# Kernel tuning notes

Measured on AMD Instinct MI355X. Metric: run time of the kernel, lower is better.

Reference implementation:

```python
import jax, jax.numpy as jnp
import numpy as np

B, T, S, D, K = 512, 49, 200, 512, 128


def setup_inputs() -> dict:
    key = jax.random.key(0)
    ks = jax.random.split(key, 8)
    return {
        "ifeature": jax.random.normal(ks[0], (B, T, D), dtype=jnp.float32),
        "tfeature_h": jax.random.normal(ks[1], (B, S, D), dtype=jnp.float32),
        "w_Dense_Vi_0": jax.random.normal(ks[2], (D, K), dtype=jnp.float32) * 0.05,
        "w_Dense_Vt_0": jax.random.normal(ks[3], (D, K), dtype=jnp.float32) * 0.05,
        "w_Dense_Pi_0": jax.random.normal(ks[4], (2 * K, 1), dtype=jnp.float32) * 0.05,
        "b_Dense_Pi_0": jnp.zeros((T,), dtype=jnp.float32),
        "w_Dense_Vi_1": jax.random.normal(ks[5], (D, K), dtype=jnp.float32) * 0.05,
        "w_Dense_Vt_1": jax.random.normal(ks[6], (D, K), dtype=jnp.float32) * 0.05,
        "w_Dense_Pi_1": jax.random.normal(ks[7], (2 * K, 1), dtype=jnp.float32) * 0.05,
        "b_Dense_Pi_1": jnp.zeros((S,), dtype=jnp.float32),
    }


def reference(ifeature, tfeature_h, w_Dense_Vi_0, w_Dense_Vt_0, w_Dense_Pi_0,
              b_Dense_Pi_0, w_Dense_Vi_1, w_Dense_Vt_1, w_Dense_Pi_1, b_Dense_Pi_1):
    # tfeature: mean-pooled text, [B, D]
    tfeature = jnp.mean(tfeature_h, axis=1)

    # --- attention over image regions (title_len) ---
    w_Vi_0 = jnp.einsum('btd,dk->btk', ifeature, w_Dense_Vi_0)          # [B,T,K]
    w_Vt_0 = (tfeature @ w_Dense_Vt_0)[:, None, :]                      # [B,1,K] broadcast to T
    Hi = jnp.tanh(jnp.concatenate(
        [w_Vi_0, jnp.broadcast_to(w_Vt_0, w_Vi_0.shape)], axis=-1))     # [B,T,2K]
    Hi_w_b = jnp.einsum('btk,k->bt', Hi, w_Dense_Pi_0[:, 0]) + b_Dense_Pi_0
    Pi = jax.nn.softmax(Hi_w_b, axis=-1)                                # [B,T]
    Vi = jnp.einsum('bt,btd->bd', Pi, ifeature)                         # attended image feature

    # --- attention over text tokens (seq_len) ---
    w_Vi_1 = (Vi @ w_Dense_Vi_1)[:, None, :]                            # [B,1,K]
    w_Vt_1 = jnp.einsum('bsd,dk->bsk', tfeature_h, w_Dense_Vt_1)        # [B,S,K]
    Ht = jnp.tanh(jnp.concatenate(
        [jnp.broadcast_to(w_Vi_1, w_Vt_1.shape), w_Vt_1], axis=-1))     # [B,S,2K]
    Ht_b = jnp.einsum('bsk,k->bs', Ht, w_Dense_Pi_1[:, 0]) + b_Dense_Pi_1
    Pt = jax.nn.softmax(Ht_b, axis=-1)                                  # [B,S]

    # NOTE: original call() returns Pt_Vt (weighted tokens), not the pooled Vt.
    Pt_Vt = Pt[:, :, None] * tfeature_h                                 # [B,S,D]
    return Pt_Vt
```

## Files before the change

kernel.cpp:

```cpp
#include <hip/hip_runtime.h>
#include <math.h>

#define BB 512
#define SS 200
#define DD 512
#define KK 128

typedef __attribute__((ext_vector_type(8))) short bf16x8;
typedef __attribute__((ext_vector_type(4))) float f32x4;

__device__ inline unsigned short f2bf(float f) {
    union { float f; unsigned int u; } v; v.f = f;
    unsigned int r = v.u + 0x7FFFu + ((v.u >> 16) & 1u);
    return (unsigned short)(r >> 16);
}

__device__ inline bf16x8 pack8(const float4& a, const float4& b) {
    bf16x8 p;
    p[0] = (short)f2bf(a.x); p[1] = (short)f2bf(a.y);
    p[2] = (short)f2bf(a.z); p[3] = (short)f2bf(a.w);
    p[4] = (short)f2bf(b.x); p[5] = (short)f2bf(b.y);
    p[6] = (short)f2bf(b.z); p[7] = (short)f2bf(b.w);
    return p;
}

__global__ void wt_kernel(const float* __restrict__ W, unsigned short* __restrict__ Wt) {
    int i = blockIdx.x * 256 + threadIdx.x;
    int col = i >> 9, d = i & 511;
    Wt[i] = f2bf(W[d * KK + col]);
}

__global__ __launch_bounds__(512, 4) void fused_kernel(
    const float* __restrict__ tfh,
    const unsigned short* __restrict__ Wt,
    const float* __restrict__ wpk,
    const float* __restrict__ bias,
    float* __restrict__ out)
{
    __shared__ unsigned short Bs[2][KK][40];
    __shared__ float logit_s[256];
    __shared__ float Pt[SS];
    __shared__ float wpart[8];

    int tid = threadIdx.x;
    int w   = tid >> 6;
    int l   = tid & 63;
    int l15 = l & 15;
    int g   = l >> 4;
    int b   = blockIdx.x;
    const float* Ab = tfh + (size_t)b * SS * DD;

    int row0 = w * 32 + l15;
    int row1 = row0 + 16;
    bool v0 = row0 < SS, v1 = row1 < SS;
    const float* a0 = Ab + (size_t)row0 * DD + g * 8;
    const float* a1 = Ab + (size_t)row1 * DD + g * 8;

    int brow = tid >> 2;
    int bcol = (tid & 3) * 8;
    const unsigned short* bp = Wt + (size_t)brow * DD + bcol;

    f32x4 acc[2][8];
    #pragma unroll
    for (int m = 0; m < 2; ++m)
        #pragma unroll
        for (int n = 0; n < 8; ++n) acc[m][n] = (f32x4){0.f, 0.f, 0.f, 0.f};

    float wv[8];
    #pragma unroll
    for (int n = 0; n < 8; ++n) wv[n] = wpk[n * 16 + l15];

    const float4 fz = make_float4(0.f, 0.f, 0.f, 0.f);

    float4 cA00 = v0 ? *(const float4*)(a0)     : fz;
    float4 cA01 = v0 ? *(const float4*)(a0 + 4) : fz;
    float4 cA10 = v1 ? *(const float4*)(a1)     : fz;
    float4 cA11 = v1 ? *(const float4*)(a1 + 4) : fz;
    *(bf16x8*)&Bs[0][brow][bcol] = *(const bf16x8*)(bp);
    __syncthreads();

    #pragma unroll 2
    for (int t = 0; t < 16; ++t) {
        int p = t & 1;
        float4 nA00, nA01, nA10, nA11;
        bf16x8 nB;
        if (t < 15) {
            int d = (t + 1) * 32;
            nA00 = v0 ? *(const float4*)(a0 + d)     : fz;
            nA01 = v0 ? *(const float4*)(a0 + d + 4) : fz;
            nA10 = v1 ? *(const float4*)(a1 + d)     : fz;
            nA11 = v1 ? *(const float4*)(a1 + d + 4) : fz;
            nB   = *(const bf16x8*)(bp + d);
        }
        bf16x8 af0 = pack8(cA00, cA01);
        bf16x8 af1 = pack8(cA10, cA11);
        #pragma unroll
        for (int n = 0; n < 8; ++n) {
            bf16x8 bfv = *(const bf16x8*)&Bs[p][n * 16 + l15][g * 8];
            acc[0][n] = __builtin_amdgcn_mfma_f32_16x16x32_bf16(af0, bfv, acc[0][n], 0, 0, 0);
            acc[1][n] = __builtin_amdgcn_mfma_f32_16x16x32_bf16(af1, bfv, acc[1][n], 0, 0, 0);
        }
        if (t < 15) *(bf16x8*)&Bs[p ^ 1][brow][bcol] = nB;
        __syncthreads();
        cA00 = nA00; cA01 = nA01; cA10 = nA10; cA11 = nA11;
    }

    float rs[2][4];
    #pragma unroll
    for (int m = 0; m < 2; ++m)
        #pragma unroll
        for (int r = 0; r < 4; ++r) rs[m][r] = 0.f;
    #pragma unroll
    for (int m = 0; m < 2; ++m)
        #pragma unroll
        for (int n = 0; n < 8; ++n)
            #pragma unroll
            for (int r = 0; r < 4; ++r)
                rs[m][r] += tanhf(acc[m][n][r]) * wv[n];
    #pragma unroll
    for (int m = 0; m < 2; ++m)
        #pragma unroll
        for (int r = 0; r < 4; ++r) {
            float v = rs[m][r];
            v += __shfl_xor(v, 1, 64);
            v += __shfl_xor(v, 2, 64);
            v += __shfl_xor(v, 4, 64);
            v += __shfl_xor(v, 8, 64);
            rs[m][r] = v;
        }
    if (l15 == 0) {
        #pragma unroll
        for (int m = 0; m < 2; ++m)
            #pragma unroll
            for (int r = 0; r < 4; ++r) {
                int srow = w * 32 + m * 16 + g * 4 + r;
                if (srow < SS) logit_s[srow] = rs[m][r] + bias[srow];
            }
    }
    __syncthreads();

    float v = (tid < SS) ? logit_s[tid] : -INFINITY;
    float m = v;
    #pragma unroll
    for (int off = 32; off > 0; off >>= 1) m = fmaxf(m, __shfl_xor(m, off, 64));
    if (l == 0) wpart[w] = m;
    __syncthreads();
    m = -INFINITY;
    #pragma unroll
    for (int i = 0; i < 8; ++i) m = fmaxf(m, wpart[i]);
    float e = (tid < SS) ? expf(v - m) : 0.f;
    float ssum = e;
    #pragma unroll
    for (int off = 32; off > 0; off >>= 1) ssum += __shfl_xor(ssum, off, 64);
    __syncthreads();
    if (l == 0) wpart[w] = ssum;
    __syncthreads();
    ssum = 0.f;
    #pragma unroll
    for (int i = 0; i < 8; ++i) ssum += wpart[i];
    if (tid < SS) Pt[tid] = e / ssum;
    __syncthreads();

    const float4* src = (const float4*)Ab;
    float4*       dst = (float4*)(out + (size_t)b * SS * DD);
    const int n4 = SS * DD / 4;
    for (int i = tid; i < n4; i += 512) {
        float p = Pt[i >> 7];
        float4 x = src[i];
        x.x *= p; x.y *= p; x.z *= p; x.w *= p;
        dst[i] = x;
    }
}

extern "C" void kernel_launch(void* const* d_in, const int* in_sizes, int n_in,
                              void* d_out, int out_size, void* d_ws, size_t ws_size,
                              hipStream_t stream) {
    const float* tfh   = (const float*)d_in[1];
    const float* wVt1  = (const float*)d_in[7];
    const float* wp1   = (const float*)d_in[8];
    const float* bias1 = (const float*)d_in[9];
    float* out = (float*)d_out;

    unsigned short* Wt = (unsigned short*)d_ws;

    wt_kernel<<<KK * DD / 256, 256, 0, stream>>>(wVt1, Wt);
    fused_kernel<<<BB, 512, 0, stream>>>(tfh, Wt, wp1 + KK, bias1, out);
}
```

Measured before the change: 141.1 us.

## Pre-swizzle weights into MFMA fragment order and load B directly from global

Result: slower. 153.1 us (+8.5%).

```diff
diff --git a/kernel.cpp b/kernel.cpp
--- a/kernel.cpp
+++ b/kernel.cpp
@@ -24,20 +24,24 @@
     return p;
 }
 
-__global__ void wt_kernel(const float* __restrict__ W, unsigned short* __restrict__ Wt) {
+__global__ void wt_kernel(const float* __restrict__ W, unsigned short* __restrict__ Wt2) {
     int i = blockIdx.x * 256 + threadIdx.x;
-    int col = i >> 9, d = i & 511;
-    Wt[i] = f2bf(W[d * KK + col]);
+    int j = i & 7;
+    int l = (i >> 3) & 63;
+    int n = (i >> 9) & 7;
+    int t = i >> 12;
+    int k = n * 16 + (l & 15);
+    int d = t * 32 + (l >> 4) * 8 + j;
+    Wt2[i] = f2bf(W[d * KK + k]);
 }
 
 __global__ __launch_bounds__(512, 4) void fused_kernel(
     const float* __restrict__ tfh,
-    const unsigned short* __restrict__ Wt,
+    const unsigned short* __restrict__ Wt2,
     const float* __restrict__ wpk,
     const float* __restrict__ bias,
     float* __restrict__ out)
 {
-    __shared__ unsigned short Bs[2][KK][40];
     __shared__ float logit_s[256];
     __shared__ float Pt[SS];
     __shared__ float wpart[8];
@@ -55,20 +59,13 @@
     bool v0 = row0 < SS, v1 = row1 < SS;
     const float* a0 = Ab + (size_t)row0 * DD + g * 8;
     const float* a1 = Ab + (size_t)row1 * DD + g * 8;
-
-    int brow = tid >> 2;
-    int bcol = (tid & 3) * 8;
-    const unsigned short* bp = Wt + (size_t)brow * DD + bcol;
+    const unsigned short* bp = Wt2 + (size_t)l * 8;
 
     f32x4 acc[2][8];
     #pragma unroll
     for (int m = 0; m < 2; ++m)
         #pragma unroll
         for (int n = 0; n < 8; ++n) acc[m][n] = (f32x4){0.f, 0.f, 0.f, 0.f};
-
-    float wv[8];
-    #pragma unroll
-    for (int n = 0; n < 8; ++n) wv[n] = wpk[n * 16 + l15];
 
     const float4 fz = make_float4(0.f, 0.f, 0.f, 0.f);
 
@@ -76,34 +73,54 @@
     float4 cA01 = v0 ? *(const float4*)(a0 + 4) : fz;
     float4 cA10 = v1 ? *(const float4*)(a1)     : fz;
     float4 cA11 = v1 ? *(const float4*)(a1 + 4) : fz;
-    *(bf16x8*)&Bs[0][brow][bcol] = *(const bf16x8*)(bp);
-    __syncthreads();
 
     #pragma unroll 2
     for (int t = 0; t < 16; ++t) {
-        int p = t & 1;
         float4 nA00, nA01, nA10, nA11;
-        bf16x8 nB;
         if (t < 15) {
             int d = (t + 1) * 32;
             nA00 = v0 ? *(const float4*)(a0 + d)     : fz;
             nA01 = v0 ? *(const float4*)(a0 + d + 4) : fz;
             nA10 = v1 ? *(const float4*)(a1 + d)     : fz;
             nA11 = v1 ? *(const float4*)(a1 + d + 4) : fz;
-            nB   = *(const bf16x8*)(bp + d);
         }
         bf16x8 af0 = pack8(cA00, cA01);
         bf16x8 af1 = pack8(cA10, cA11);
-        #pragma unroll
-        for (int n = 0; n < 8; ++n) {
-            bf16x8 bfv = *(const bf16x8*)&Bs[p][n * 16 + l15][g * 8];
-            acc[0][n] = __builtin_amdgcn_mfma_f32_16x16x32_bf16(af0, bfv, acc[0][n], 0, 0, 0);
-            acc[1][n] = __builtin_amdgcn_mfma_f32_16x16x32_bf16(af1, bfv, acc[1][n], 0, 0, 0);
-        }
-        if (t < 15) *(bf16x8*)&Bs[p ^ 1][brow][bcol] = nB;
-        __syncthreads();
+        const unsigned short* bt = bp + (size_t)t * (8 * 64 * 8);
+        {
+            bf16x8 b0 = *(const bf16x8*)(bt);
+            bf16x8 b1 = *(const bf16x8*)(bt + 1 * 512);
+            bf16x8 b2 = *(const bf16x8*)(bt + 2 * 512);
+            bf16x8 b3 = *(const bf16x8*)(bt + 3 * 512);
+            acc[0][0] = __builtin_amdgcn_mfma_f32_16x16x32_bf16(af0, b0, acc[0][0], 0, 0, 0);
+            acc[1][0] = __builtin_amdgcn_mfma_f32_16x16x32_bf16(af1, b0, acc[1][0], 0, 0, 0);
+            acc[0][1] = __builtin_amdgcn_mfma_f32_16x16x32_bf16(af0, b1, acc[0][1], 0, 0, 0);
+            acc[1][1] = __builtin_amdgcn_mfma_f32_16x16x32_bf16(af1, b1, acc[1][1], 0, 0, 0);
+            acc[0][2] = __builtin_amdgcn_mfma_f32_16x16x32_bf16(af0, b2, acc[0][2], 0, 0, 0);
+            acc[1][2] = __builtin_amdgcn_mfma_f32_16x16x32_bf16(af1, b2, acc[1][2], 0, 0, 0);
+            acc[0][3] = __builtin_amdgcn_mfma_f32_16x16x32_bf16(af0, b3, acc[0][3], 0, 0, 0);
+            acc[1][3] = __builtin_amdgcn_mfma_f32_16x16x32_bf16(af1, b3, acc[1][3], 0, 0, 0);
+        }
+        {
+            bf16x8 b4 = *(const bf16x8*)(bt + 4 * 512);
+            bf16x8 b5 = *(const bf16x8*)(bt + 5 * 512);
+            bf16x8 b6 = *(const bf16x8*)(bt + 6 * 512);
+            bf16x8 b7 = *(const bf16x8*)(bt + 7 * 512);
+            acc[0][4] = __builtin_amdgcn_mfma_f32_16x16x32_bf16(af0, b4, acc[0][4], 0, 0, 0);
+            acc[1][4] = __builtin_amdgcn_mfma_f32_16x16x32_bf16(af1, b4, acc[1][4], 0, 0, 0);
+            acc[0][5] = __builtin_amdgcn_mfma_f32_16x16x32_bf16(af0, b5, acc[0][5], 0, 0, 0);
+            acc[1][5] = __builtin_amdgcn_mfma_f32_16x16x32_bf16(af1, b5, acc[1][5], 0, 0, 0);
+            acc[0][6] = __builtin_amdgcn_mfma_f32_16x16x32_bf16(af0, b6, acc[0][6], 0, 0, 0);
+            acc[1][6] = __builtin_amdgcn_mfma_f32_16x16x32_bf16(af1, b6, acc[1][6], 0, 0, 0);
+            acc[0][7] = __builtin_amdgcn_mfma_f32_16x16x32_bf16(af0, b7, acc[0][7], 0, 0, 0);
+            acc[1][7] = __builtin_amdgcn_mfma_f32_16x16x32_bf16(af1, b7, acc[1][7], 0, 0, 0);
+        }
         cA00 = nA00; cA01 = nA01; cA10 = nA10; cA11 = nA11;
     }
+
+    float wv[8];
+    #pragma unroll
+    for (int n = 0; n < 8; ++n) wv[n] = wpk[n * 16 + l15];
 
     float rs[2][4];
     #pragma unroll
@@ -181,8 +198,8 @@
     const float* bias1 = (const float*)d_in[9];
     float* out = (float*)d_out;
 
-    unsigned short* Wt = (unsigned short*)d_ws;
-
-    wt_kernel<<<KK * DD / 256, 256, 0, stream>>>(wVt1, Wt);
-    fused_kernel<<<BB, 512, 0, stream>>>(tfh, Wt, wp1 + KK, bias1, out);
-}
+    unsigned short* Wt2 = (unsigned short*)d_ws;
+
+    wt_kernel<<<(16 * 8 * 64 * 8) / 256, 256, 0, stream>>>(wVt1, Wt2);
+    fused_kernel<<<BB, 512, 0, stream>>>(tfh, Wt2, wp1 + KK, bias1, out);
+}
```
